# Optimization experiments

Hardware: AMD Instinct MI355X
Metric: run time of the kernel (lower is better)

Reference implementation:

```python
import jax, jax.numpy as jnp
import numpy as np

N_NODES = 100000
N_EDGES = 1600000
IN_DIM, HID_DIM, OUT_DIM = 128, 64, 16
BN_EPS = 1e-5


def sage_conv(x, edge_index, W_l, b_l, W_r):
    # PyG SAGEConv (aggr='mean'): out = lin_l(mean_j x_j) + lin_r(x_i)
    src, dst = edge_index[0], edge_index[1]
    msgs = x[src]                                   # [E, F] gather
    sums = jax.ops.segment_sum(msgs, dst, num_segments=N_NODES)      # [N, F]
    cnt = jax.ops.segment_sum(jnp.ones((src.shape[0],), x.dtype), dst,
                              num_segments=N_NODES)                  # [N]
    agg = sums / jnp.maximum(cnt, 1.0)[:, None]     # mean; 0 for isolated nodes
    return agg @ W_l.T + b_l + x @ W_r.T


def batchnorm(x, gamma, beta):
    # BatchNorm1d in training mode: normalize over the node (batch) axis
    mean = jnp.mean(x, axis=0)
    var = jnp.var(x, axis=0)
    return (x - mean) * jax.lax.rsqrt(var + BN_EPS) * gamma + beta


def setup_inputs() -> dict:
    key = jax.random.key(0)
    ks = jax.random.split(key, 8)
    x = jax.random.normal(ks[0], (N_NODES, IN_DIM), dtype=jnp.float32)
    edge_index = jax.random.randint(ks[1], (2, N_EDGES), 0, N_NODES)
    s1 = 1.0 / np.sqrt(IN_DIM)
    s2 = 1.0 / np.sqrt(HID_DIM)
    return {
        "x": x,
        "edge_index": edge_index,
        "W1_l": jax.random.uniform(ks[2], (HID_DIM, IN_DIM), minval=-s1, maxval=s1),
        "b1": jnp.zeros((HID_DIM,), jnp.float32),
        "W1_r": jax.random.uniform(ks[3], (HID_DIM, IN_DIM), minval=-s1, maxval=s1),
        "bn_gamma": jnp.ones((HID_DIM,), jnp.float32),
        "bn_beta": jnp.zeros((HID_DIM,), jnp.float32),
        "W2_l": jax.random.uniform(ks[4], (OUT_DIM, HID_DIM), minval=-s2, maxval=s2),
        "b2": jnp.zeros((OUT_DIM,), jnp.float32),
        "W2_r": jax.random.uniform(ks[5], (OUT_DIM, HID_DIM), minval=-s2, maxval=s2),
    }


def reference(x, edge_index, W1_l, b1, W1_r, bn_gamma, bn_beta, W2_l, b2, W2_r):
    h = sage_conv(x, edge_index, W1_l, b1, W1_r)
    h = jax.nn.relu(batchnorm(h, bn_gamma, bn_beta))
    return sage_conv(h, edge_index, W2_l, b2, W2_r)
```

## Files before the change

kernel.cpp:

```cpp
#include <hip/hip_runtime.h>

#define NN 100000
#define NE 1600000
#define NPB 128
#define NBK 782
#define EPB 16384
#define NPART 98
#define NCVT 18
#define NT64 1563
#define NT128 782
#define CAP 4096

#define OFF_H      0
#define OFF_GCNT   0
#define OFF_GOFS   80000
#define OFF_W1BF   160000
#define OFF_YL     6400000
#define OFF_YR     9600000
#define OFF_EBUF   12800000
#define OFF_HIST   14400000
#define OFF_BSTART 14500000
#define OFF_BNACC  14500800
#define OFF_W2BF   14500928

typedef __attribute__((ext_vector_type(8))) short bf16x8;
typedef __attribute__((ext_vector_type(4))) float f32x4;

__device__ __forceinline__ ushort f2bf(float f) {
  unsigned u = __float_as_uint(f);
  u += 0x7fffu + ((u >> 16) & 1);
  return (ushort)(u >> 16);
}
#define BFLO(u) __uint_as_float(((u) & 0xffffu) << 16)
#define BFHI(u) __uint_as_float((u) & 0xffff0000u)

__global__ __launch_bounds__(1024) void k_bcnt2(const int* __restrict__ ei,
                                                int* __restrict__ gcnt,
                                                const float* __restrict__ W1l,
                                                const float* __restrict__ W1r,
                                                const float* __restrict__ W2l,
                                                const float* __restrict__ W2r,
                                                ushort* __restrict__ w1bf,
                                                ushort* __restrict__ w2bf) {
  const int tid = threadIdx.x;
  if (blockIdx.x >= NPART) {
    int i = (blockIdx.x - NPART) * 1024 + tid;
    if (i < 16384) {
      w1bf[i] = f2bf(i < 8192 ? W1l[i] : W1r[i - 8192]);
    } else if (i < 16384 + 2048) {
      int j = i - 16384;
      w2bf[j] = f2bf(j < 1024 ? W2l[j] : W2r[j - 1024]);
    }
    return;
  }
  __shared__ int cnt[NBK];
  for (int i = tid; i < NBK; i += 1024) cnt[i] = 0;
  __syncthreads();
  int e0 = blockIdx.x * EPB;
  int e1 = min(e0 + EPB, NE);
  for (int base = e0; base < e1; base += 4096) {
    int e = base + tid * 4;
    if (e + 3 < e1) {
      int4 vd = *(const int4*)&ei[NE + e];
      atomicAdd(&cnt[vd.x >> 7], 1);
      atomicAdd(&cnt[vd.y >> 7], 1);
      atomicAdd(&cnt[vd.z >> 7], 1);
      atomicAdd(&cnt[vd.w >> 7], 1);
    } else {
      for (int k = e; k < e1; ++k) atomicAdd(&cnt[ei[NE + k] >> 7], 1);
    }
  }
  __syncthreads();
  for (int b = tid; b < NBK; b += 1024)
    gcnt[blockIdx.x * NBK + b] = cnt[b];
}

__global__ __launch_bounds__(1024) void k_bprep(const int* __restrict__ gcnt,
                                                int* __restrict__ bstart,
                                                int* __restrict__ gofs) {
  __shared__ int sd[1024];
  int t = threadIdx.x;
  int total = 0;
  if (t < NBK)
    for (int blk = 0; blk < NPART; ++blk) total += gcnt[blk * NBK + t];
  sd[t] = total;
  __syncthreads();
  for (int off = 1; off < 1024; off <<= 1) {
    int u = (t >= off) ? sd[t - off] : 0;
    __syncthreads();
    sd[t] += u;
    __syncthreads();
  }
  if (t < NBK) {
    int run = sd[t] - total;
    bstart[t] = run;
    for (int blk = 0; blk < NPART; ++blk) {
      gofs[blk * NBK + t] = run;
      run += gcnt[blk * NBK + t];
    }
  }
  if (t == 0) bstart[NBK] = NE;
}

__global__ __launch_bounds__(512) void k_pg(const int* __restrict__ ei,
                                            const int* __restrict__ gofs,
                                            int* __restrict__ ebuf,
                                            const float* __restrict__ x,
                                            const ushort* __restrict__ w1bf,
                                            ushort* __restrict__ yl,
                                            ushort* __restrict__ yr) {
  __shared__ ushort smem[128 * 136];
  const int tid = threadIdx.x;

  if (blockIdx.x < NPART) {
    int* gstart = (int*)smem;
    int* cur = gstart + NBK;
    for (int i = tid; i < NBK; i += 512) {
      gstart[i] = gofs[blockIdx.x * NBK + i];
      cur[i] = 0;
    }
    __syncthreads();
    int e0 = blockIdx.x * EPB;
    int e1 = min(e0 + EPB, NE);
    for (int base = e0; base < e1; base += 2048) {
      int e = base + tid * 4;
      if (e + 3 < e1) {
        int4 vs = *(const int4*)&ei[e];
        int4 vd = *(const int4*)&ei[NE + e];
        int b0 = vd.x >> 7, b1 = vd.y >> 7, b2 = vd.z >> 7, b3 = vd.w >> 7;
        int r0 = atomicAdd(&cur[b0], 1);
        int r1 = atomicAdd(&cur[b1], 1);
        int r2 = atomicAdd(&cur[b2], 1);
        int r3 = atomicAdd(&cur[b3], 1);
        ebuf[gstart[b0] + r0] = (vs.x << 7) | (vd.x & 127);
        ebuf[gstart[b1] + r1] = (vs.y << 7) | (vd.y & 127);
        ebuf[gstart[b2] + r2] = (vs.z << 7) | (vd.z & 127);
        ebuf[gstart[b3] + r3] = (vs.w << 7) | (vd.w & 127);
      } else {
        for (int k = e; k < e1; ++k) {
          int s = ei[k], d = ei[NE + k];
          int b = d >> 7;
          int r = atomicAdd(&cur[b], 1);
          ebuf[gstart[b] + r] = (s << 7) | (d & 127);
        }
      }
    }
    return;
  }

  ushort* xs = smem;
  const int n0 = (blockIdx.x - NPART) * 128;

  for (int i = tid; i < 128 * 32; i += 512) {
    int r = i >> 5, c = i & 31;
    int n = n0 + r;
    float4 v = (n < NN) ? *(const float4*)&x[(size_t)n * 128 + c * 4]
                        : make_float4(0.f, 0.f, 0.f, 0.f);
    *(ushort4*)&xs[r * 136 + c * 4] = make_ushort4(f2bf(v.x), f2bf(v.y), f2bf(v.z), f2bf(v.w));
  }
  __syncthreads();

  const int w = tid >> 6, l = tid & 63;
  const int col = l & 15, kb = l >> 4;

  f32x4 acc[8];
#pragma unroll
  for (int nt = 0; nt < 8; ++nt) acc[nt] = (f32x4){0.f, 0.f, 0.f, 0.f};

#pragma unroll
  for (int kc = 0; kc < 4; ++kc) {
    int koff = kc * 32 + kb * 8;
    bf16x8 b = *(const bf16x8*)&w1bf[(w * 16 + col) * 128 + koff];
#pragma unroll
    for (int nt = 0; nt < 8; ++nt) {
      bf16x8 a = *(const bf16x8*)&xs[(nt * 16 + col) * 136 + koff];
      acc[nt] = __builtin_amdgcn_mfma_f32_16x16x32_bf16(a, b, acc[nt], 0, 0, 0);
    }
  }

  __syncthreads();
  const int outc = w * 16 + col;
#pragma unroll
  for (int nt = 0; nt < 8; ++nt)
#pragma unroll
    for (int r = 0; r < 4; ++r)
      xs[(nt * 16 + kb * 4 + r) * 136 + outc] = f2bf(acc[nt][r]);
  __syncthreads();

  for (int i = tid; i < 2048; i += 512) {
    int row = i >> 4, seg = i & 15;
    int n = n0 + row;
    if (n < NN) {
      uint4 v = *(const uint4*)&xs[row * 136 + seg * 8];
      if (seg < 8) *(uint4*)&yl[(size_t)n * 64 + seg * 8] = v;
      else         *(uint4*)&yr[(size_t)n * 64 + (seg - 8) * 8] = v;
    }
  }
}

__global__ __launch_bounds__(512) void k_agg1c(int* __restrict__ ebuf,
                                               const int* __restrict__ bstart,
                                               int* __restrict__ hist,
                                               const ushort* __restrict__ yl,
                                               const ushort* __restrict__ yr,
                                               const float* __restrict__ b1,
                                               float* __restrict__ h,
                                               float* __restrict__ bnacc) {
  __shared__ int raw[CAP];
  __shared__ int srt[CAP];
  __shared__ int sd[128], deg[128], offx[128], cursor[128];
  __shared__ float bnWs[8][64], bnWq[8][64];
  const int tid = threadIdx.x;
  const int b = blockIdx.x;
  const int node0 = b << 7;
  const int nnode = min(NPB, NN - node0);
  const int kstart = bstart[b];
  const int T = min(bstart[b + 1] - kstart, CAP);

  if (tid < 128) deg[tid] = 0;
  __syncthreads();
  for (int i = tid; i < T; i += 512) {
    int e = ebuf[kstart + i];
    raw[i] = e;
    atomicAdd(&deg[e & 127], 1);
  }
  __syncthreads();
  if (tid < 128) sd[tid] = deg[tid];
  __syncthreads();
  for (int o = 1; o < 128; o <<= 1) {
    int v = (tid < 128 && tid >= o) ? sd[tid - o] : 0;
    __syncthreads();
    if (tid < 128) sd[tid] += v;
    __syncthreads();
  }
  if (tid < 128) {
    int s = sd[tid] - deg[tid];
    offx[tid] = s;
    cursor[tid] = s;
    if (tid < nnode) hist[node0 + tid] = deg[tid];
  }
  __syncthreads();

  for (int i = tid; i < T; i += 512) {
    int e = raw[i];
    int slot = atomicAdd(&cursor[e & 127], 1);
    srt[slot] = e >> 7;
  }
  __syncthreads();

  for (int i = tid; i < T; i += 512) ebuf[kstart + i] = srt[i];

  const int g = tid >> 3, f8 = tid & 7;
  float s[8] = {}, q[8] = {};
#pragma unroll
  for (int rep = 0; rep < 2; ++rep) {
    int dl = g + rep * 64;
    if (dl < nnode) {
      int st = offx[dl], d = deg[dl];
      float a[8] = {};
      int k = st, ke = st + d;
      for (; k + 3 < ke; k += 4) {
        int s0 = srt[k], s1 = srt[k + 1], s2 = srt[k + 2], s3 = srt[k + 3];
        uint4 v0 = *(const uint4*)&yl[(size_t)s0 * 64 + f8 * 8];
        uint4 v1 = *(const uint4*)&yl[(size_t)s1 * 64 + f8 * 8];
        uint4 v2 = *(const uint4*)&yl[(size_t)s2 * 64 + f8 * 8];
        uint4 v3 = *(const uint4*)&yl[(size_t)s3 * 64 + f8 * 8];
        a[0] += (BFLO(v0.x) + BFLO(v1.x)) + (BFLO(v2.x) + BFLO(v3.x));
        a[1] += (BFHI(v0.x) + BFHI(v1.x)) + (BFHI(v2.x) + BFHI(v3.x));
        a[2] += (BFLO(v0.y) + BFLO(v1.y)) + (BFLO(v2.y) + BFLO(v3.y));
        a[3] += (BFHI(v0.y) + BFHI(v1.y)) + (BFHI(v2.y) + BFHI(v3.y));
        a[4] += (BFLO(v0.z) + BFLO(v1.z)) + (BFLO(v2.z) + BFLO(v3.z));
        a[5] += (BFHI(v0.z) + BFHI(v1.z)) + (BFHI(v2.z) + BFHI(v3.z));
        a[6] += (BFLO(v0.w) + BFLO(v1.w)) + (BFLO(v2.w) + BFLO(v3.w));
        a[7] += (BFHI(v0.w) + BFHI(v1.w)) + (BFHI(v2.w) + BFHI(v3.w));
      }
      for (; k < ke; ++k) {
        int s0 = srt[k];
        uint4 v0 = *(const uint4*)&yl[(size_t)s0 * 64 + f8 * 8];
        a[0] += BFLO(v0.x); a[1] += BFHI(v0.x);
        a[2] += BFLO(v0.y); a[3] += BFHI(v0.y);
        a[4] += BFLO(v0.z); a[5] += BFHI(v0.z);
        a[6] += BFLO(v0.w); a[7] += BFHI(v0.w);
      }
      int node = node0 + dl;
      float invc = 1.0f / fmaxf((float)d, 1.0f);
      uint4 rv = *(const uint4*)&yr[(size_t)node * 64 + f8 * 8];
      float4 bv0 = *(const float4*)&b1[f8 * 8];
      float4 bv1 = *(const float4*)&b1[f8 * 8 + 4];
      float hv[8];
      hv[0] = a[0] * invc + bv0.x + BFLO(rv.x);
      hv[1] = a[1] * invc + bv0.y + BFHI(rv.x);
      hv[2] = a[2] * invc + bv0.z + BFLO(rv.y);
      hv[3] = a[3] * invc + bv0.w + BFHI(rv.y);
      hv[4] = a[4] * invc + bv1.x + BFLO(rv.z);
      hv[5] = a[5] * invc + bv1.y + BFHI(rv.z);
      hv[6] = a[6] * invc + bv1.z + BFLO(rv.w);
      hv[7] = a[7] * invc + bv1.w + BFHI(rv.w);
      *(float4*)&h[(size_t)node * 64 + f8 * 8]     = make_float4(hv[0], hv[1], hv[2], hv[3]);
      *(float4*)&h[(size_t)node * 64 + f8 * 8 + 4] = make_float4(hv[4], hv[5], hv[6], hv[7]);
#pragma unroll
      for (int j = 0; j < 8; ++j) { s[j] += hv[j]; q[j] += hv[j] * hv[j]; }
    }
  }

#pragma unroll
  for (int j = 0; j < 8; ++j) {
    s[j] += __shfl_xor(s[j], 8);  s[j] += __shfl_xor(s[j], 16); s[j] += __shfl_xor(s[j], 32);
    q[j] += __shfl_xor(q[j], 8);  q[j] += __shfl_xor(q[j], 16); q[j] += __shfl_xor(q[j], 32);
  }
  const int w = tid >> 6, lane = tid & 63;
  if (lane < 8) {
#pragma unroll
    for (int j = 0; j < 8; ++j) {
      bnWs[w][lane * 8 + j] = s[j];
      bnWq[w][lane * 8 + j] = q[j];
    }
  }
  __syncthreads();
  if (tid < 64) {
    float S = 0.f, Q = 0.f;
#pragma unroll
    for (int ww = 0; ww < 8; ++ww) { S += bnWs[ww][tid]; Q += bnWq[ww][tid]; }
    atomicAdd(&bnacc[tid], S);
    atomicAdd(&bnacc[64 + tid], Q);
  }
}

__global__ __launch_bounds__(256) void k_layer2m(const float* __restrict__ h,
                                                 const ushort* __restrict__ w2bf,
                                                 const float* __restrict__ b2,
                                                 const float* __restrict__ bnacc,
                                                 const float* __restrict__ gamma,
                                                 const float* __restrict__ beta,
                                                 ushort* __restrict__ zl,
                                                 float* __restrict__ zr) {
  __shared__ ushort hs[64 * 72];
  __shared__ float sc[64], sh[64];
  const int tid = threadIdx.x;
  const int n0 = blockIdx.x * 64;

  if (tid < 64) {
    float mean = bnacc[tid] * (1.0f / NN);
    float var = bnacc[64 + tid] * (1.0f / NN) - mean * mean;
    float scv = gamma[tid] * rsqrtf(var + 1e-5f);
    sc[tid] = scv;
    sh[tid] = beta[tid] - mean * scv;
  }
  __syncthreads();

  for (int i = tid; i < 64 * 16; i += 256) {
    int r = i >> 4, c = i & 15;
    int n = n0 + r;
    float4 v = (n < NN) ? *(const float4*)&h[(size_t)n * 64 + c * 4]
                        : make_float4(0.f, 0.f, 0.f, 0.f);
    float4 o;
    o.x = fmaxf(v.x * sc[c * 4 + 0] + sh[c * 4 + 0], 0.f);
    o.y = fmaxf(v.y * sc[c * 4 + 1] + sh[c * 4 + 1], 0.f);
    o.z = fmaxf(v.z * sc[c * 4 + 2] + sh[c * 4 + 2], 0.f);
    o.w = fmaxf(v.w * sc[c * 4 + 3] + sh[c * 4 + 3], 0.f);
    *(ushort4*)&hs[r * 72 + c * 4] = make_ushort4(f2bf(o.x), f2bf(o.y), f2bf(o.z), f2bf(o.w));
  }
  __syncthreads();

  const int w = tid >> 6, l = tid & 63;
  const int col = l & 15, kb = l >> 4;

  f32x4 acc[2] = {(f32x4){0.f, 0.f, 0.f, 0.f}, (f32x4){0.f, 0.f, 0.f, 0.f}};
#pragma unroll
  for (int kc = 0; kc < 2; ++kc) {
    int koff = kc * 32 + kb * 8;
    bf16x8 a = *(const bf16x8*)&hs[(w * 16 + col) * 72 + koff];
    bf16x8 b0 = *(const bf16x8*)&w2bf[col * 64 + koff];
    bf16x8 b1v = *(const bf16x8*)&w2bf[(16 + col) * 64 + koff];
    acc[0] = __builtin_amdgcn_mfma_f32_16x16x32_bf16(a, b0, acc[0], 0, 0, 0);
    acc[1] = __builtin_amdgcn_mfma_f32_16x16x32_bf16(a, b1v, acc[1], 0, 0, 0);
  }

#pragma unroll
  for (int r = 0; r < 4; ++r) {
    int n = n0 + w * 16 + kb * 4 + r;
    if (n < NN) {
      zl[(size_t)n * 16 + col] = f2bf(acc[0][r]);
      zr[(size_t)n * 16 + col] = acc[1][r] + b2[col];
    }
  }
}

__global__ __launch_bounds__(512) void k_agg2c(const int* __restrict__ ebuf,
                                               const int* __restrict__ bstart,
                                               const int* __restrict__ hist,
                                               const ushort* __restrict__ zl,
                                               const float* __restrict__ zr,
                                               float* __restrict__ out) {
  __shared__ int elist[CAP];
  __shared__ int sd[128], deg[128], offx[128];
  const int tid = threadIdx.x;
  const int b = blockIdx.x;
  const int node0 = b << 7;
  const int nnode = min(NPB, NN - node0);
  const int kstart = bstart[b];
  const int T = min(bstart[b + 1] - kstart, CAP);

  for (int i = tid; i < T; i += 512) elist[i] = ebuf[kstart + i];
  if (tid < 128) {
    int d = (tid < nnode) ? hist[node0 + tid] : 0;
    deg[tid] = d;
    sd[tid] = d;
  }
  __syncthreads();
  for (int o = 1; o < 128; o <<= 1) {
    int v = (tid < 128 && tid >= o) ? sd[tid - o] : 0;
    __syncthreads();
    if (tid < 128) sd[tid] += v;
    __syncthreads();
  }
  if (tid < 128) offx[tid] = sd[tid] - deg[tid];
  __syncthreads();

  const int g = tid >> 3, f8 = tid & 7;
#pragma unroll
  for (int rep = 0; rep < 2; ++rep) {
    int dl = g + rep * 64;
    if (dl < nnode) {
      int st = offx[dl], d = deg[dl];
      float a0 = 0.f, a1 = 0.f;
      int k = st, ke = st + d;
      for (; k + 3 < ke; k += 4) {
        int s0 = elist[k], s1 = elist[k + 1], s2 = elist[k + 2], s3 = elist[k + 3];
        unsigned v0 = *(const unsigned*)&zl[(size_t)s0 * 16 + f8 * 2];
        unsigned v1 = *(const unsigned*)&zl[(size_t)s1 * 16 + f8 * 2];
        unsigned v2 = *(const unsigned*)&zl[(size_t)s2 * 16 + f8 * 2];
        unsigned v3 = *(const unsigned*)&zl[(size_t)s3 * 16 + f8 * 2];
        a0 += (BFLO(v0) + BFLO(v1)) + (BFLO(v2) + BFLO(v3));
        a1 += (BFHI(v0) + BFHI(v1)) + (BFHI(v2) + BFHI(v3));
      }
      for (; k < ke; ++k) {
        unsigned v0 = *(const unsigned*)&zl[(size_t)elist[k] * 16 + f8 * 2];
        a0 += BFLO(v0);
        a1 += BFHI(v0);
      }
      int node = node0 + dl;
      float invc = 1.0f / fmaxf((float)d, 1.0f);
      size_t base = (size_t)node * 16 + f8 * 2;
      out[base]     = a0 * invc + zr[base];
      out[base + 1] = a1 * invc + zr[base + 1];
    }
  }
}

extern "C" void kernel_launch(void* const* d_in, const int* in_sizes, int n_in,
                              void* d_out, int out_size, void* d_ws, size_t ws_size,
                              hipStream_t stream) {
  const float* x     = (const float*)d_in[0];
  const int*   ei    = (const int*)d_in[1];
  const float* W1l   = (const float*)d_in[2];
  const float* b1    = (const float*)d_in[3];
  const float* W1r   = (const float*)d_in[4];
  const float* gamma = (const float*)d_in[5];
  const float* beta  = (const float*)d_in[6];
  const float* W2l   = (const float*)d_in[7];
  const float* b2    = (const float*)d_in[8];
  const float* W2r   = (const float*)d_in[9];
  float* out = (float*)d_out;
  float* ws  = (float*)d_ws;

  float*  hbuf   = ws + OFF_H;
  int*    gcnt   = (int*)(ws + OFF_GCNT);
  int*    gofs   = (int*)(ws + OFF_GOFS);
  ushort* w1bf   = (ushort*)(ws + OFF_W1BF);
  ushort* yl     = (ushort*)(ws + OFF_YL);
  ushort* yr     = (ushort*)(ws + OFF_YR);
  ushort* zl     = (ushort*)(ws + OFF_YL);
  float*  zr     = ws + OFF_YR;
  int*    ebuf   = (int*)(ws + OFF_EBUF);
  int*    hist   = (int*)(ws + OFF_HIST);
  int*    bstart = (int*)(ws + OFF_BSTART);
  float*  bnacc  = ws + OFF_BNACC;
  ushort* w2bf   = (ushort*)(ws + OFF_W2BF);

  hipMemsetAsync(bnacc, 0, 128 * sizeof(float), stream);

  k_bcnt2<<<NPART + NCVT, 1024, 0, stream>>>(ei, gcnt, W1l, W1r, W2l, W2r, w1bf, w2bf);
  k_bprep<<<1, 1024, 0, stream>>>(gcnt, bstart, gofs);
  k_pg<<<NPART + NT128, 512, 0, stream>>>(ei, gofs, ebuf, x, w1bf, yl, yr);
  k_agg1c<<<NBK, 512, 0, stream>>>(ebuf, bstart, hist, yl, yr, b1, hbuf, bnacc);
  k_layer2m<<<NT64, 256, 0, stream>>>(hbuf, w2bf, b2, bnacc, gamma, beta, zl, zr);
  k_agg2c<<<NBK, 512, 0, stream>>>(ebuf, bstart, hist, zl, zr, out);
}
```

Measured before the change: 132.7 us.

## Fuse bucket counting into partition kernel with fixed-capacity slots and bf16 hidden

Drops the separate count and prefix-scan kernels. Each partition block now counts its edges locally and reserves space in fixed-capacity per-bucket slots through global atomics. Weight conversion to bf16 moves inline into the GEMM kernels, the layer-1 hidden activations are stored as bf16 instead of fp32, and both aggregation loops interleave two nodes per thread group to expose more memory parallelism. This removes two launches and a serial scan, and halves hidden-activation traffic. The cost is that edges beyond a bucket's fixed capacity are silently dropped, edge order within buckets becomes nondeterministic, and the bf16 hidden adds rounding error.

```diff
diff --git a/kernel.cpp b/kernel.cpp
--- a/kernel.cpp
+++ b/kernel.cpp
@@ -6,22 +6,17 @@
 #define NBK 782
 #define EPB 16384
 #define NPART 98
-#define NCVT 18
+#define NT128 782
 #define NT64 1563
-#define NT128 782
-#define CAP 4096
+#define CAPSLOT 2432
 
 #define OFF_H      0
-#define OFF_GCNT   0
-#define OFF_GOFS   80000
-#define OFF_W1BF   160000
-#define OFF_YL     6400000
-#define OFF_YR     9600000
-#define OFF_EBUF   12800000
-#define OFF_HIST   14400000
-#define OFF_BSTART 14500000
-#define OFF_BNACC  14500800
-#define OFF_W2BF   14500928
+#define OFF_YL     3200000
+#define OFF_YR     6400000
+#define OFF_EBUF   9600000
+#define OFF_HIST   11501824
+#define OFF_BCURP  11601824
+#define OFF_BNACC  11614336
 
 typedef __attribute__((ext_vector_type(8))) short bf16x8;
 typedef __attribute__((ext_vector_type(4))) float f32x4;
@@ -33,115 +28,77 @@
 }
 #define BFLO(u) __uint_as_float(((u) & 0xffffu) << 16)
 #define BFHI(u) __uint_as_float((u) & 0xffff0000u)
-
-__global__ __launch_bounds__(1024) void k_bcnt2(const int* __restrict__ ei,
-                                                int* __restrict__ gcnt,
-                                                const float* __restrict__ W1l,
-                                                const float* __restrict__ W1r,
-                                                const float* __restrict__ W2l,
-                                                const float* __restrict__ W2r,
-                                                ushort* __restrict__ w1bf,
-                                                ushort* __restrict__ w2bf) {
-  const int tid = threadIdx.x;
-  if (blockIdx.x >= NPART) {
-    int i = (blockIdx.x - NPART) * 1024 + tid;
-    if (i < 16384) {
-      w1bf[i] = f2bf(i < 8192 ? W1l[i] : W1r[i - 8192]);
-    } else if (i < 16384 + 2048) {
-      int j = i - 16384;
-      w2bf[j] = f2bf(j < 1024 ? W2l[j] : W2r[j - 1024]);
-    }
-    return;
-  }
-  __shared__ int cnt[NBK];
-  for (int i = tid; i < NBK; i += 1024) cnt[i] = 0;
-  __syncthreads();
-  int e0 = blockIdx.x * EPB;
-  int e1 = min(e0 + EPB, NE);
-  for (int base = e0; base < e1; base += 4096) {
-    int e = base + tid * 4;
-    if (e + 3 < e1) {
-      int4 vd = *(const int4*)&ei[NE + e];
-      atomicAdd(&cnt[vd.x >> 7], 1);
-      atomicAdd(&cnt[vd.y >> 7], 1);
-      atomicAdd(&cnt[vd.z >> 7], 1);
-      atomicAdd(&cnt[vd.w >> 7], 1);
-    } else {
-      for (int k = e; k < e1; ++k) atomicAdd(&cnt[ei[NE + k] >> 7], 1);
-    }
-  }
-  __syncthreads();
-  for (int b = tid; b < NBK; b += 1024)
-    gcnt[blockIdx.x * NBK + b] = cnt[b];
-}
-
-__global__ __launch_bounds__(1024) void k_bprep(const int* __restrict__ gcnt,
-                                                int* __restrict__ bstart,
-                                                int* __restrict__ gofs) {
-  __shared__ int sd[1024];
-  int t = threadIdx.x;
-  int total = 0;
-  if (t < NBK)
-    for (int blk = 0; blk < NPART; ++blk) total += gcnt[blk * NBK + t];
-  sd[t] = total;
-  __syncthreads();
-  for (int off = 1; off < 1024; off <<= 1) {
-    int u = (t >= off) ? sd[t - off] : 0;
-    __syncthreads();
-    sd[t] += u;
-    __syncthreads();
-  }
-  if (t < NBK) {
-    int run = sd[t] - total;
-    bstart[t] = run;
-    for (int blk = 0; blk < NPART; ++blk) {
-      gofs[blk * NBK + t] = run;
-      run += gcnt[blk * NBK + t];
-    }
-  }
-  if (t == 0) bstart[NBK] = NE;
+#define ACC8(A, v) { A[0] += BFLO(v.x); A[1] += BFHI(v.x); A[2] += BFLO(v.y); A[3] += BFHI(v.y); \
+                     A[4] += BFLO(v.z); A[5] += BFHI(v.z); A[6] += BFLO(v.w); A[7] += BFHI(v.w); }
+
+__device__ __forceinline__ bf16x8 packrow(const float* p) {
+  float4 a = *(const float4*)p, b = *(const float4*)(p + 4);
+  bf16x8 r;
+  r[0] = (short)f2bf(a.x); r[1] = (short)f2bf(a.y);
+  r[2] = (short)f2bf(a.z); r[3] = (short)f2bf(a.w);
+  r[4] = (short)f2bf(b.x); r[5] = (short)f2bf(b.y);
+  r[6] = (short)f2bf(b.z); r[7] = (short)f2bf(b.w);
+  return r;
 }
 
 __global__ __launch_bounds__(512) void k_pg(const int* __restrict__ ei,
-                                            const int* __restrict__ gofs,
+                                            int* __restrict__ bcurp,
                                             int* __restrict__ ebuf,
                                             const float* __restrict__ x,
-                                            const ushort* __restrict__ w1bf,
+                                            const float* __restrict__ W1l,
+                                            const float* __restrict__ W1r,
                                             ushort* __restrict__ yl,
                                             ushort* __restrict__ yr) {
   __shared__ ushort smem[128 * 136];
   const int tid = threadIdx.x;
 
   if (blockIdx.x < NPART) {
-    int* gstart = (int*)smem;
+    int* cnt = (int*)smem;
+    int* gstart = cnt + NBK;
     int* cur = gstart + NBK;
-    for (int i = tid; i < NBK; i += 512) {
-      gstart[i] = gofs[blockIdx.x * NBK + i];
-      cur[i] = 0;
-    }
+    for (int i = tid; i < NBK; i += 512) cnt[i] = 0;
     __syncthreads();
     int e0 = blockIdx.x * EPB;
     int e1 = min(e0 + EPB, NE);
+    for (int base = e0; base < e1; base += 2048) {
+      int e = base + tid * 4;
+      if (e + 3 < e1) {
+        int4 vd = *(const int4*)&ei[NE + e];
+        atomicAdd(&cnt[vd.x >> 7], 1);
+        atomicAdd(&cnt[vd.y >> 7], 1);
+        atomicAdd(&cnt[vd.z >> 7], 1);
+        atomicAdd(&cnt[vd.w >> 7], 1);
+      } else {
+        for (int k = e; k < e1; ++k) atomicAdd(&cnt[ei[NE + k] >> 7], 1);
+      }
+    }
+    __syncthreads();
+    for (int b = tid; b < NBK; b += 512) {
+      int c = cnt[b];
+      gstart[b] = c ? atomicAdd(&bcurp[b * 16], c) : 0;
+      cur[b] = 0;
+    }
+    __syncthreads();
     for (int base = e0; base < e1; base += 2048) {
       int e = base + tid * 4;
       if (e + 3 < e1) {
         int4 vs = *(const int4*)&ei[e];
         int4 vd = *(const int4*)&ei[NE + e];
         int b0 = vd.x >> 7, b1 = vd.y >> 7, b2 = vd.z >> 7, b3 = vd.w >> 7;
-        int r0 = atomicAdd(&cur[b0], 1);
-        int r1 = atomicAdd(&cur[b1], 1);
-        int r2 = atomicAdd(&cur[b2], 1);
-        int r3 = atomicAdd(&cur[b3], 1);
-        ebuf[gstart[b0] + r0] = (vs.x << 7) | (vd.x & 127);
-        ebuf[gstart[b1] + r1] = (vs.y << 7) | (vd.y & 127);
-        ebuf[gstart[b2] + r2] = (vs.z << 7) | (vd.z & 127);
-        ebuf[gstart[b3] + r3] = (vs.w << 7) | (vd.w & 127);
+        int r0 = gstart[b0] + atomicAdd(&cur[b0], 1);
+        int r1 = gstart[b1] + atomicAdd(&cur[b1], 1);
+        int r2 = gstart[b2] + atomicAdd(&cur[b2], 1);
+        int r3 = gstart[b3] + atomicAdd(&cur[b3], 1);
+        if (r0 < CAPSLOT) ebuf[b0 * CAPSLOT + r0] = (vs.x << 7) | (vd.x & 127);
+        if (r1 < CAPSLOT) ebuf[b1 * CAPSLOT + r1] = (vs.y << 7) | (vd.y & 127);
+        if (r2 < CAPSLOT) ebuf[b2 * CAPSLOT + r2] = (vs.z << 7) | (vd.z & 127);
+        if (r3 < CAPSLOT) ebuf[b3 * CAPSLOT + r3] = (vs.w << 7) | (vd.w & 127);
       } else {
         for (int k = e; k < e1; ++k) {
           int s = ei[k], d = ei[NE + k];
           int b = d >> 7;
-          int r = atomicAdd(&cur[b], 1);
-          ebuf[gstart[b] + r] = (s << 7) | (d & 127);
+          int r = gstart[b] + atomicAdd(&cur[b], 1);
+          if (r < CAPSLOT) ebuf[b * CAPSLOT + r] = (s << 7) | (d & 127);
         }
       }
     }
@@ -162,6 +119,8 @@
 
   const int w = tid >> 6, l = tid & 63;
   const int col = l & 15, kb = l >> 4;
+  const int outc = w * 16 + col;
+  const float* wrow = (outc < 64) ? &W1l[outc * 128] : &W1r[(outc - 64) * 128];
 
   f32x4 acc[8];
 #pragma unroll
@@ -170,7 +129,7 @@
 #pragma unroll
   for (int kc = 0; kc < 4; ++kc) {
     int koff = kc * 32 + kb * 8;
-    bf16x8 b = *(const bf16x8*)&w1bf[(w * 16 + col) * 128 + koff];
+    bf16x8 b = packrow(&wrow[koff]);
 #pragma unroll
     for (int nt = 0; nt < 8; ++nt) {
       bf16x8 a = *(const bf16x8*)&xs[(nt * 16 + col) * 136 + koff];
@@ -179,7 +138,6 @@
   }
 
   __syncthreads();
-  const int outc = w * 16 + col;
 #pragma unroll
   for (int nt = 0; nt < 8; ++nt)
 #pragma unroll
@@ -199,23 +157,23 @@
 }
 
 __global__ __launch_bounds__(512) void k_agg1c(int* __restrict__ ebuf,
-                                               const int* __restrict__ bstart,
+                                               const int* __restrict__ bcurp,
                                                int* __restrict__ hist,
                                                const ushort* __restrict__ yl,
                                                const ushort* __restrict__ yr,
                                                const float* __restrict__ b1,
-                                               float* __restrict__ h,
+                                               ushort* __restrict__ h,
                                                float* __restrict__ bnacc) {
-  __shared__ int raw[CAP];
-  __shared__ int srt[CAP];
+  __shared__ int raw[CAPSLOT];
+  __shared__ int srt[CAPSLOT];
   __shared__ int sd[128], deg[128], offx[128], cursor[128];
   __shared__ float bnWs[8][64], bnWq[8][64];
   const int tid = threadIdx.x;
   const int b = blockIdx.x;
   const int node0 = b << 7;
   const int nnode = min(NPB, NN - node0);
-  const int kstart = bstart[b];
-  const int T = min(bstart[b + 1] - kstart, CAP);
+  const int kstart = b * CAPSLOT;
+  const int T = min(bcurp[b * 16], CAPSLOT);
 
   if (tid < 128) deg[tid] = 0;
   __syncthreads();
@@ -251,53 +209,69 @@
   for (int i = tid; i < T; i += 512) ebuf[kstart + i] = srt[i];
 
   const int g = tid >> 3, f8 = tid & 7;
+  float A0[8] = {}, A1[8] = {};
+  const bool v0 = g < nnode, v1 = (g + 64) < nnode;
+  int k0 = v0 ? offx[g] : 0;
+  int ke0 = v0 ? k0 + deg[g] : 0;
+  int k1 = v1 ? offx[g + 64] : 0;
+  int ke1 = v1 ? k1 + deg[g + 64] : 0;
+
+  while (k0 + 1 < ke0 && k1 + 1 < ke1) {
+    int s00 = srt[k0], s01 = srt[k0 + 1], s10 = srt[k1], s11 = srt[k1 + 1];
+    uint4 u00 = *(const uint4*)&yl[(size_t)s00 * 64 + f8 * 8];
+    uint4 u01 = *(const uint4*)&yl[(size_t)s01 * 64 + f8 * 8];
+    uint4 u10 = *(const uint4*)&yl[(size_t)s10 * 64 + f8 * 8];
+    uint4 u11 = *(const uint4*)&yl[(size_t)s11 * 64 + f8 * 8];
+    ACC8(A0, u00); ACC8(A0, u01); ACC8(A1, u10); ACC8(A1, u11);
+    k0 += 2; k1 += 2;
+  }
+  for (; k0 + 1 < ke0; k0 += 2) {
+    int s00 = srt[k0], s01 = srt[k0 + 1];
+    uint4 u00 = *(const uint4*)&yl[(size_t)s00 * 64 + f8 * 8];
+    uint4 u01 = *(const uint4*)&yl[(size_t)s01 * 64 + f8 * 8];
+    ACC8(A0, u00); ACC8(A0, u01);
+  }
+  if (k0 < ke0) {
+    uint4 u = *(const uint4*)&yl[(size_t)srt[k0] * 64 + f8 * 8];
+    ACC8(A0, u);
+  }
+  for (; k1 + 1 < ke1; k1 += 2) {
+    int s10 = srt[k1], s11 = srt[k1 + 1];
+    uint4 u10 = *(const uint4*)&yl[(size_t)s10 * 64 + f8 * 8];
+    uint4 u11 = *(const uint4*)&yl[(size_t)s11 * 64 + f8 * 8];
+    ACC8(A1, u10); ACC8(A1, u11);
+  }
+  if (k1 < ke1) {
+    uint4 u = *(const uint4*)&yl[(size_t)srt[k1] * 64 + f8 * 8];
+    ACC8(A1, u);
+  }
+
+  const float4 bv0 = *(const float4*)&b1[f8 * 8];
+  const float4 bv1 = *(const float4*)&b1[f8 * 8 + 4];
   float s[8] = {}, q[8] = {};
 #pragma unroll
   for (int rep = 0; rep < 2; ++rep) {
     int dl = g + rep * 64;
+    float* A = rep ? A1 : A0;
     if (dl < nnode) {
-      int st = offx[dl], d = deg[dl];
-      float a[8] = {};
-      int k = st, ke = st + d;
-      for (; k + 3 < ke; k += 4) {
-        int s0 = srt[k], s1 = srt[k + 1], s2 = srt[k + 2], s3 = srt[k + 3];
-        uint4 v0 = *(const uint4*)&yl[(size_t)s0 * 64 + f8 * 8];
-        uint4 v1 = *(const uint4*)&yl[(size_t)s1 * 64 + f8 * 8];
-        uint4 v2 = *(const uint4*)&yl[(size_t)s2 * 64 + f8 * 8];
-        uint4 v3 = *(const uint4*)&yl[(size_t)s3 * 64 + f8 * 8];
-        a[0] += (BFLO(v0.x) + BFLO(v1.x)) + (BFLO(v2.x) + BFLO(v3.x));
-        a[1] += (BFHI(v0.x) + BFHI(v1.x)) + (BFHI(v2.x) + BFHI(v3.x));
-        a[2] += (BFLO(v0.y) + BFLO(v1.y)) + (BFLO(v2.y) + BFLO(v3.y));
-        a[3] += (BFHI(v0.y) + BFHI(v1.y)) + (BFHI(v2.y) + BFHI(v3.y));
-        a[4] += (BFLO(v0.z) + BFLO(v1.z)) + (BFLO(v2.z) + BFLO(v3.z));
-        a[5] += (BFHI(v0.z) + BFHI(v1.z)) + (BFHI(v2.z) + BFHI(v3.z));
-        a[6] += (BFLO(v0.w) + BFLO(v1.w)) + (BFLO(v2.w) + BFLO(v3.w));
-        a[7] += (BFHI(v0.w) + BFHI(v1.w)) + (BFHI(v2.w) + BFHI(v3.w));
-      }
-      for (; k < ke; ++k) {
-        int s0 = srt[k];
-        uint4 v0 = *(const uint4*)&yl[(size_t)s0 * 64 + f8 * 8];
-        a[0] += BFLO(v0.x); a[1] += BFHI(v0.x);
-        a[2] += BFLO(v0.y); a[3] += BFHI(v0.y);
-        a[4] += BFLO(v0.z); a[5] += BFHI(v0.z);
-        a[6] += BFLO(v0.w); a[7] += BFHI(v0.w);
-      }
       int node = node0 + dl;
-      float invc = 1.0f / fmaxf((float)d, 1.0f);
+      float invc = 1.0f / fmaxf((float)deg[dl], 1.0f);
       uint4 rv = *(const uint4*)&yr[(size_t)node * 64 + f8 * 8];
-      float4 bv0 = *(const float4*)&b1[f8 * 8];
-      float4 bv1 = *(const float4*)&b1[f8 * 8 + 4];
       float hv[8];
-      hv[0] = a[0] * invc + bv0.x + BFLO(rv.x);
-      hv[1] = a[1] * invc + bv0.y + BFHI(rv.x);
-      hv[2] = a[2] * invc + bv0.z + BFLO(rv.y);
-      hv[3] = a[3] * invc + bv0.w + BFHI(rv.y);
-      hv[4] = a[4] * invc + bv1.x + BFLO(rv.z);
-      hv[5] = a[5] * invc + bv1.y + BFHI(rv.z);
-      hv[6] = a[6] * invc + bv1.z + BFLO(rv.w);
-      hv[7] = a[7] * invc + bv1.w + BFHI(rv.w);
-      *(float4*)&h[(size_t)node * 64 + f8 * 8]     = make_float4(hv[0], hv[1], hv[2], hv[3]);
-      *(float4*)&h[(size_t)node * 64 + f8 * 8 + 4] = make_float4(hv[4], hv[5], hv[6], hv[7]);
+      hv[0] = A[0] * invc + bv0.x + BFLO(rv.x);
+      hv[1] = A[1] * invc + bv0.y + BFHI(rv.x);
+      hv[2] = A[2] * invc + bv0.z + BFLO(rv.y);
+      hv[3] = A[3] * invc + bv0.w + BFHI(rv.y);
+      hv[4] = A[4] * invc + bv1.x + BFLO(rv.z);
+      hv[5] = A[5] * invc + bv1.y + BFHI(rv.z);
+      hv[6] = A[6] * invc + bv1.z + BFLO(rv.w);
+      hv[7] = A[7] * invc + bv1.w + BFHI(rv.w);
+      uint4 hp;
+      hp.x = (unsigned)f2bf(hv[0]) | ((unsigned)f2bf(hv[1]) << 16);
+      hp.y = (unsigned)f2bf(hv[2]) | ((unsigned)f2bf(hv[3]) << 16);
+      hp.z = (unsigned)f2bf(hv[4]) | ((unsigned)f2bf(hv[5]) << 16);
+      hp.w = (unsigned)f2bf(hv[6]) | ((unsigned)f2bf(hv[7]) << 16);
+      *(uint4*)&h[(size_t)node * 64 + f8 * 8] = hp;
 #pragma unroll
       for (int j = 0; j < 8; ++j) { s[j] += hv[j]; q[j] += hv[j] * hv[j]; }
     }
@@ -326,8 +300,9 @@
   }
 }
 
-__global__ __launch_bounds__(256) void k_layer2m(const float* __restrict__ h,
-                                                 const ushort* __restrict__ w2bf,
+__global__ __launch_bounds__(256) void k_layer2m(const ushort* __restrict__ h,
+                                                 const float* __restrict__ W2l,
+                                                 const float* __restrict__ W2r,
                                                  const float* __restrict__ b2,
                                                  const float* __restrict__ bnacc,
                                                  const float* __restrict__ gamma,
@@ -348,30 +323,42 @@
   }
   __syncthreads();
 
-  for (int i = tid; i < 64 * 16; i += 256) {
-    int r = i >> 4, c = i & 15;
+  for (int i = tid; i < 64 * 8; i += 256) {
+    int r = i >> 3, seg = i & 7;
     int n = n0 + r;
-    float4 v = (n < NN) ? *(const float4*)&h[(size_t)n * 64 + c * 4]
-                        : make_float4(0.f, 0.f, 0.f, 0.f);
-    float4 o;
-    o.x = fmaxf(v.x * sc[c * 4 + 0] + sh[c * 4 + 0], 0.f);
-    o.y = fmaxf(v.y * sc[c * 4 + 1] + sh[c * 4 + 1], 0.f);
-    o.z = fmaxf(v.z * sc[c * 4 + 2] + sh[c * 4 + 2], 0.f);
-    o.w = fmaxf(v.w * sc[c * 4 + 3] + sh[c * 4 + 3], 0.f);
-    *(ushort4*)&hs[r * 72 + c * 4] = make_ushort4(f2bf(o.x), f2bf(o.y), f2bf(o.z), f2bf(o.w));
+    uint4 v = (n < NN) ? *(const uint4*)&h[(size_t)n * 64 + seg * 8]
+                       : make_uint4(0, 0, 0, 0);
+    const float* scp = &sc[seg * 8];
+    const float* shp = &sh[seg * 8];
+    float o0 = fmaxf(BFLO(v.x) * scp[0] + shp[0], 0.f);
+    float o1 = fmaxf(BFHI(v.x) * scp[1] + shp[1], 0.f);
+    float o2 = fmaxf(BFLO(v.y) * scp[2] + shp[2], 0.f);
+    float o3 = fmaxf(BFHI(v.y) * scp[3] + shp[3], 0.f);
+    float o4 = fmaxf(BFLO(v.z) * scp[4] + shp[4], 0.f);
+    float o5 = fmaxf(BFHI(v.z) * scp[5] + shp[5], 0.f);
+    float o6 = fmaxf(BFLO(v.w) * scp[6] + shp[6], 0.f);
+    float o7 = fmaxf(BFHI(v.w) * scp[7] + shp[7], 0.f);
+    uint4 p;
+    p.x = (unsigned)f2bf(o0) | ((unsigned)f2bf(o1) << 16);
+    p.y = (unsigned)f2bf(o2) | ((unsigned)f2bf(o3) << 16);
+    p.z = (unsigned)f2bf(o4) | ((unsigned)f2bf(o5) << 16);
+    p.w = (unsigned)f2bf(o6) | ((unsigned)f2bf(o7) << 16);
+    *(uint4*)&hs[r * 72 + seg * 8] = p;
   }
   __syncthreads();
 
   const int w = tid >> 6, l = tid & 63;
   const int col = l & 15, kb = l >> 4;
+  const float* w2row0 = &W2l[col * 64];
+  const float* w2row1 = &W2r[col * 64];
 
   f32x4 acc[2] = {(f32x4){0.f, 0.f, 0.f, 0.f}, (f32x4){0.f, 0.f, 0.f, 0.f}};
 #pragma unroll
   for (int kc = 0; kc < 2; ++kc) {
     int koff = kc * 32 + kb * 8;
     bf16x8 a = *(const bf16x8*)&hs[(w * 16 + col) * 72 + koff];
-    bf16x8 b0 = *(const bf16x8*)&w2bf[col * 64 + koff];
-    bf16x8 b1v = *(const bf16x8*)&w2bf[(16 + col) * 64 + koff];
+    bf16x8 b0 = packrow(&w2row0[koff]);
+    bf16x8 b1v = packrow(&w2row1[koff]);
     acc[0] = __builtin_amdgcn_mfma_f32_16x16x32_bf16(a, b0, acc[0], 0, 0, 0);
     acc[1] = __builtin_amdgcn_mfma_f32_16x16x32_bf16(a, b1v, acc[1], 0, 0, 0);
   }
@@ -387,19 +374,19 @@
 }
 
 __global__ __launch_bounds__(512) void k_agg2c(const int* __restrict__ ebuf,
-                                               const int* __restrict__ bstart,
+                                               const int* __restrict__ bcurp,
                                                const int* __restrict__ hist,
                                                const ushort* __restrict__ zl,
                                                const float* __restrict__ zr,
                                                float* __restrict__ out) {
-  __shared__ int elist[CAP];
+  __shared__ int elist[CAPSLOT];
   __shared__ int sd[128], deg[128], offx[128];
   const int tid = threadIdx.x;
   const int b = blockIdx.x;
   const int node0 = b << 7;
   const int nnode = min(NPB, NN - node0);
-  const int kstart = bstart[b];
-  const int T = min(bstart[b + 1] - kstart, CAP);
+  const int kstart = b * CAPSLOT;
+  const int T = min(bcurp[b * 16], CAPSLOT);
 
   for (int i = tid; i < T; i += 512) elist[i] = ebuf[kstart + i];
   if (tid < 128) {
@@ -418,33 +405,44 @@
   __syncthreads();
 
   const int g = tid >> 3, f8 = tid & 7;
-#pragma unroll
-  for (int rep = 0; rep < 2; ++rep) {
-    int dl = g + rep * 64;
-    if (dl < nnode) {
-      int st = offx[dl], d = deg[dl];
-      float a0 = 0.f, a1 = 0.f;
-      int k = st, ke = st + d;
-      for (; k + 3 < ke; k += 4) {
-        int s0 = elist[k], s1 = elist[k + 1], s2 = elist[k + 2], s3 = elist[k + 3];
-        unsigned v0 = *(const unsigned*)&zl[(size_t)s0 * 16 + f8 * 2];
-        unsigned v1 = *(const unsigned*)&zl[(size_t)s1 * 16 + f8 * 2];
-        unsigned v2 = *(const unsigned*)&zl[(size_t)s2 * 16 + f8 * 2];
-        unsigned v3 = *(const unsigned*)&zl[(size_t)s3 * 16 + f8 * 2];
-        a0 += (BFLO(v0) + BFLO(v1)) + (BFLO(v2) + BFLO(v3));
-        a1 += (BFHI(v0) + BFHI(v1)) + (BFHI(v2) + BFHI(v3));
-      }
-      for (; k < ke; ++k) {
-        unsigned v0 = *(const unsigned*)&zl[(size_t)elist[k] * 16 + f8 * 2];
-        a0 += BFLO(v0);
-        a1 += BFHI(v0);
-      }
-      int node = node0 + dl;
-      float invc = 1.0f / fmaxf((float)d, 1.0f);
-      size_t base = (size_t)node * 16 + f8 * 2;
-      out[base]     = a0 * invc + zr[base];
-      out[base + 1] = a1 * invc + zr[base + 1];
-    }
+  float a00 = 0.f, a01 = 0.f, a10 = 0.f, a11 = 0.f;
+  const bool v0 = g < nnode, v1 = (g + 64) < nnode;
+  int k0 = v0 ? offx[g] : 0;
+  int ke0 = v0 ? k0 + deg[g] : 0;
+  int k1 = v1 ? offx[g + 64] : 0;
+  int ke1 = v1 ? k1 + deg[g + 64] : 0;
+
+  while (k0 + 1 < ke0 && k1 + 1 < ke1) {
+    unsigned u00 = *(const unsigned*)&zl[(size_t)elist[k0] * 16 + f8 * 2];
+    unsigned u01 = *(const unsigned*)&zl[(size_t)elist[k0 + 1] * 16 + f8 * 2];
+    unsigned u10 = *(const unsigned*)&zl[(size_t)elist[k1] * 16 + f8 * 2];
+    unsigned u11 = *(const unsigned*)&zl[(size_t)elist[k1 + 1] * 16 + f8 * 2];
+    a00 += BFLO(u00) + BFLO(u01); a01 += BFHI(u00) + BFHI(u01);
+    a10 += BFLO(u10) + BFLO(u11); a11 += BFHI(u10) + BFHI(u11);
+    k0 += 2; k1 += 2;
+  }
+  for (; k0 < ke0; ++k0) {
+    unsigned u = *(const unsigned*)&zl[(size_t)elist[k0] * 16 + f8 * 2];
+    a00 += BFLO(u); a01 += BFHI(u);
+  }
+  for (; k1 < ke1; ++k1) {
+    unsigned u = *(const unsigned*)&zl[(size_t)elist[k1] * 16 + f8 * 2];
+    a10 += BFLO(u); a11 += BFHI(u);
+  }
+
+  if (v0) {
+    int node = node0 + g;
+    float invc = 1.0f / fmaxf((float)deg[g], 1.0f);
+    size_t base = (size_t)node * 16 + f8 * 2;
+    out[base]     = a00 * invc + zr[base];
+    out[base + 1] = a01 * invc + zr[base + 1];
+  }
+  if (v1) {
+    int node = node0 + g + 64;
+    float invc = 1.0f / fmaxf((float)deg[g + 64], 1.0f);
+    size_t base = (size_t)node * 16 + f8 * 2;
+    out[base]     = a10 * invc + zr[base];
+    out[base + 1] = a11 * invc + zr[base + 1];
   }
 }
 
@@ -464,26 +462,20 @@
   float* out = (float*)d_out;
   float* ws  = (float*)d_ws;
 
-  float*  hbuf   = ws + OFF_H;
-  int*    gcnt   = (int*)(ws + OFF_GCNT);
-  int*    gofs   = (int*)(ws + OFF_GOFS);
-  ushort* w1bf   = (ushort*)(ws + OFF_W1BF);
+  ushort* hbf    = (ushort*)(ws + OFF_H);
   ushort* yl     = (ushort*)(ws + OFF_YL);
   ushort* yr     = (ushort*)(ws + OFF_YR);
   ushort* zl     = (ushort*)(ws + OFF_YL);
   float*  zr     = ws + OFF_YR;
   int*    ebuf   = (int*)(ws + OFF_EBUF);
   int*    hist   = (int*)(ws + OFF_HIST);
-  int*    bstart = (int*)(ws + OFF_BSTART);
+  int*    bcurp  = (int*)(ws + OFF_BCURP);
   float*  bnacc  = ws + OFF_BNACC;
-  ushort* w2bf   = (ushort*)(ws + OFF_W2BF);
-
-  hipMemsetAsync(bnacc, 0, 128 * sizeof(float), stream);
-
-  k_bcnt2<<<NPART + NCVT, 1024, 0, stream>>>(ei, gcnt, W1l, W1r, W2l, W2r, w1bf, w2bf);
-  k_bprep<<<1, 1024, 0, stream>>>(gcnt, bstart, gofs);
-  k_pg<<<NPART + NT128, 512, 0, stream>>>(ei, gofs, ebuf, x, w1bf, yl, yr);
-  k_agg1c<<<NBK, 512, 0, stream>>>(ebuf, bstart, hist, yl, yr, b1, hbuf, bnacc);
-  k_layer2m<<<NT64, 256, 0, stream>>>(hbuf, w2bf, b2, bnacc, gamma, beta, zl, zr);
-  k_agg2c<<<NBK, 512, 0, stream>>>(ebuf, bstart, hist, zl, zr, out);
-}
+
+  hipMemsetAsync(bcurp, 0, (12512 + 128) * sizeof(int), stream);
+
+  k_pg<<<NPART + NT128, 512, 0, stream>>>(ei, bcurp, ebuf, x, W1l, W1r, yl, yr);
+  k_agg1c<<<NBK, 512, 0, stream>>>(ebuf, bcurp, hist, yl, yr, b1, hbf, bnacc);
+  k_layer2m<<<NT64, 256, 0, stream>>>(hbf, W2l, W2r, b2, bnacc, gamma, beta, zl, zr);
+  k_agg2c<<<NBK, 512, 0, stream>>>(ebuf, bcurp, hist, zl, zr, out);
+}
```

Result: no change. 131.1 us (-1.2%).
